# Kernel optimization log

Hardware: AMD Instinct MI355X
Metric: run time of the kernel (lower is better)

## Reference

```python
import jax, jax.numpy as jnp
import numpy as np

B, DIM, H, W = 2, 256, 32, 32
HALF, DI, DS, DTR = DIM // 2, 256, 16, 8
DEPTH, K1 = 2, 4


def _ln(x, w, b, eps=1e-5):
    m = jnp.mean(x, -1, keepdims=True)
    v = jnp.var(x, -1, keepdims=True)
    return (x - m) * jax.lax.rsqrt(v + eps) * w + b


def _selective_scan(dA, dBu, C):
    # dA, dBu: (N, L, D, S); C: (N, L, S) -> y: (N, L, D)
    def step(h, ab):
        a, b = ab
        h = a * h + b
        return h, h
    h0 = jnp.zeros((dA.shape[0],) + dA.shape[2:], dA.dtype)
    _, hs = jax.lax.scan(step, h0, (jnp.moveaxis(dA, 1, 0), jnp.moveaxis(dBu, 1, 0)))
    return jnp.einsum('lnds,nls->nld', hs, C)


def _mamba_block(xs, ln_w, ln_b, in_w, cw, cb, xw, dtw, dtb, Alog, Dp, ow):
    # xs: (B, L, HALF); canonical Mamba-1 block, pre-LN residual
    Lq = xs.shape[1]
    h = _ln(xs, ln_w, ln_b)
    u, z = jnp.split(h @ in_w, 2, axis=-1)  # (B,L,DI) each
    up = jnp.pad(u, ((0, 0), (K1 - 1, 0), (0, 0)))  # causal depthwise conv1d
    u = sum(up[:, k:k + Lq, :] * cw[:, k] for k in range(K1)) + cb
    u = jax.nn.silu(u)
    dbc = u @ xw
    dtr, Bm, Cm = jnp.split(dbc, [DTR, DTR + DS], axis=-1)
    dt = jax.nn.softplus(dtr @ dtw + dtb)  # (B,L,DI)
    A = -jnp.exp(Alog)  # (DI,DS)
    dA = jnp.exp(dt[..., None] * A)
    dBu = (dt * u)[..., None] * Bm[:, :, None, :]
    y = _selective_scan(dA, dBu, Cm) + u * Dp
    return xs + (y * jax.nn.silu(z)) @ ow


def _vss_block(x, ln_w, ln_b, in_w, cw, cb, xw, dtw, dtb, Alog, Dp, on_w, on_b, ow):
    # x: (B, HALF, H, W); VMamba SS2D block (4-direction cross-scan), pre-LN residual
    Bq, _, Hq, Wq = x.shape
    Lq = Hq * Wq
    h = _ln(x.transpose(0, 2, 3, 1), ln_w, ln_b)
    u, z = jnp.split(h @ in_w, 2, axis=-1)  # (B,H,W,DI)
    u2 = jax.lax.conv_general_dilated(u.transpose(0, 3, 1, 2), cw[:, None], (1, 1), ((1, 1), (1, 1)),
                                      feature_group_count=DI,
                                      dimension_numbers=('NCHW', 'OIHW', 'NCHW')) + cb[None, :, None, None]
    u2 = jax.nn.silu(u2)  # (B,DI,H,W)
    s0 = u2.reshape(Bq, DI, Lq)
    s1 = u2.transpose(0, 1, 3, 2).reshape(Bq, DI, Lq)
    us = jnp.stack([s0, s1, jnp.flip(s0, -1), jnp.flip(s1, -1)], 1).transpose(0, 1, 3, 2)  # (B,4,L,DI)
    dbc = jnp.einsum('bkld,kdr->bklr', us, xw)
    dtr, Bm, Cm = jnp.split(dbc, [DTR, DTR + DS], axis=-1)
    dt = jax.nn.softplus(jnp.einsum('bklr,krd->bkld', dtr, dtw) + dtb[None, :, None, :])
    A = -jnp.exp(Alog)  # (4,DI,DS)
    dA = jnp.exp(dt[..., None] * A[None, :, None])  # (B,4,L,DI,DS)
    dBu = (dt * us)[..., None] * Bm[:, :, :, None, :]
    y = _selective_scan(dA.reshape(Bq * 4, Lq, DI, DS), dBu.reshape(Bq * 4, Lq, DI, DS), Cm.reshape(Bq * 4, Lq, DS))
    y = y.reshape(Bq, 4, Lq, DI) + us * Dp[None, :, None, :]
    yt = y.transpose(0, 1, 3, 2)  # (B,4,DI,L)
    y0 = yt[:, 0]
    y1 = yt[:, 1].reshape(Bq, DI, Wq, Hq).transpose(0, 1, 3, 2).reshape(Bq, DI, Lq)
    y2 = jnp.flip(yt[:, 2], -1)
    y3 = jnp.flip(yt[:, 3], -1).reshape(Bq, DI, Wq, Hq).transpose(0, 1, 3, 2).reshape(Bq, DI, Lq)
    ym = _ln((y0 + y1 + y2 + y3).transpose(0, 2, 1), on_w, on_b)  # (B,L,DI)
    out = (ym * jax.nn.silu(z.reshape(Bq, Lq, DI))) @ ow  # (B,L,HALF)
    return x + out.reshape(Bq, Hq, Wq, HALF).transpose(0, 3, 1, 2)


def _fwd(x, proj1_w, proj1_b, proj2_w, proj2_b,
         m_ln_w, m_ln_b, m_in_w, m_conv_w, m_conv_b, m_xproj_w, m_dt_w, m_dt_b, m_Alog, m_D, m_out_w,
         v_ln_w, v_ln_b, v_in_w, v_conv_w, v_conv_b, v_xproj_w, v_dt_w, v_dt_b, v_Alog, v_D,
         v_onorm_w, v_onorm_b, v_out_w, fuse_w, fuse_b, bn_g, bn_b, bn_m, bn_v):
    Bq, _, Hq, Wq = x.shape
    Lq = Hq * Wq
    p1 = jnp.einsum('oc,bchw->bohw', proj1_w, x) + proj1_b[None, :, None, None]
    s = p1.reshape(Bq, HALF, Lq).transpose(0, 2, 1)
    for i in range(DEPTH):
        s = _mamba_block(s, m_ln_w[i], m_ln_b[i], m_in_w[i], m_conv_w[i], m_conv_b[i], m_xproj_w[i],
                         m_dt_w[i], m_dt_b[i], m_Alog[i], m_D[i], m_out_w[i])
    p1 = s.transpose(0, 2, 1).reshape(Bq, HALF, Hq, Wq)
    p2 = jnp.einsum('oc,bchw->bohw', proj2_w, x) + proj2_b[None, :, None, None]
    for i in range(DEPTH):
        p2 = _vss_block(p2, v_ln_w[i], v_ln_b[i], v_in_w[i], v_conv_w[i], v_conv_b[i], v_xproj_w[i],
                        v_dt_w[i], v_dt_b[i], v_Alog[i], v_D[i], v_onorm_w[i], v_onorm_b[i], v_out_w[i])
    xc = jnp.concatenate([p1, p2], 1)
    y = jax.lax.conv_general_dilated(xc, fuse_w, (1, 1), ((1, 1), (1, 1)),
                                     dimension_numbers=('NCHW', 'OIHW', 'NCHW')) + fuse_b[None, :, None, None]
    y = (y - bn_m[None, :, None, None]) * jax.lax.rsqrt(bn_v + 1e-5)[None, :, None, None] * bn_g[None, :, None, None] + bn_b[None, :, None, None]
    return jax.nn.relu(y)


def setup_inputs() -> dict:
    key = jax.random.key(0)
    ks = iter(jax.random.split(key, 64))
    n = lambda shape, s=0.02: jax.random.normal(next(ks), shape, jnp.float32) * s
    A_row = jnp.log(jnp.arange(1, DS + 1, dtype=jnp.float32))  # standard S4D-real init
    return {
        'x': jax.random.normal(next(ks), (B, DIM, H, W), jnp.float32),
        'proj1_w': n((HALF, DIM), 0.05), 'proj1_b': n((HALF,)),
        'proj2_w': n((HALF, DIM), 0.05), 'proj2_b': n((HALF,)),
        'm_ln_w': jnp.ones((DEPTH, HALF)), 'm_ln_b': jnp.zeros((DEPTH, HALF)),
        'm_in_w': n((DEPTH, HALF, 2 * DI)),
        'm_conv_w': n((DEPTH, DI, K1), 0.1), 'm_conv_b': n((DEPTH, DI)),
        'm_xproj_w': n((DEPTH, DI, DTR + 2 * DS)),
        'm_dt_w': n((DEPTH, DTR, DI), 0.1), 'm_dt_b': n((DEPTH, DI)),
        'm_Alog': jnp.array(jnp.broadcast_to(A_row, (DEPTH, DI, DS))),
        'm_D': jnp.ones((DEPTH, DI)),
        'm_out_w': n((DEPTH, DI, HALF)),
        'v_ln_w': jnp.ones((DEPTH, HALF)), 'v_ln_b': jnp.zeros((DEPTH, HALF)),
        'v_in_w': n((DEPTH, HALF, 2 * DI)),
        'v_conv_w': n((DEPTH, DI, 3, 3), 0.1), 'v_conv_b': n((DEPTH, DI)),
        'v_xproj_w': n((DEPTH, 4, DI, DTR + 2 * DS)),
        'v_dt_w': n((DEPTH, 4, DTR, DI), 0.1), 'v_dt_b': n((DEPTH, 4, DI)),
        'v_Alog': jnp.array(jnp.broadcast_to(A_row, (DEPTH, 4, DI, DS))),
        'v_D': jnp.ones((DEPTH, 4, DI)),
        'v_onorm_w': jnp.ones((DEPTH, DI)), 'v_onorm_b': jnp.zeros((DEPTH, DI)),
        'v_out_w': n((DEPTH, DI, HALF)),
        'fuse_w': n((DIM, DIM, 3, 3), 0.02), 'fuse_b': n((DIM,)),
        'bn_g': jnp.ones((DIM,)), 'bn_b': jnp.zeros((DIM,)),
        'bn_m': n((DIM,)), 'bn_v': jax.random.uniform(next(ks), (DIM,), jnp.float32, 0.5, 1.5),
    }


def reference(x, proj1_w, proj1_b, proj2_w, proj2_b,
              m_ln_w, m_ln_b, m_in_w, m_conv_w, m_conv_b, m_xproj_w, m_dt_w, m_dt_b, m_Alog, m_D, m_out_w,
              v_ln_w, v_ln_b, v_in_w, v_conv_w, v_conv_b, v_xproj_w, v_dt_w, v_dt_b, v_Alog, v_D,
              v_onorm_w, v_onorm_b, v_out_w, fuse_w, fuse_b, bn_g, bn_b, bn_m, bn_v):
    return _fwd(x, proj1_w, proj1_b, proj2_w, proj2_b,
                m_ln_w, m_ln_b, m_in_w, m_conv_w, m_conv_b, m_xproj_w, m_dt_w, m_dt_b, m_Alog, m_D, m_out_w,
                v_ln_w, v_ln_b, v_in_w, v_conv_w, v_conv_b, v_xproj_w, v_dt_w, v_dt_b, v_Alog, v_D,
                v_onorm_w, v_onorm_b, v_out_w, fuse_w, fuse_b, bn_g, bn_b, bn_m, bn_v)
```

## Files before the change

### kernel.cpp

```cpp
#include <hip/hip_runtime.h>
#include <math.h>

#define CH  16
#define NCH 64

typedef __attribute__((ext_vector_type(8))) short bf16x8;
typedef __attribute__((ext_vector_type(4))) float f32x4;
typedef __attribute__((ext_vector_type(4))) unsigned int u32x4;

__device__ __forceinline__ float dev_silu(float x){ return x * (1.0f/(1.0f + __expf(-x))); }
__device__ __forceinline__ float dev_softplus(float x){ return fmaxf(x,0.0f) + log1pf(__expf(-fabsf(x))); }
__device__ __forceinline__ unsigned short dev_bf16(float f){
    unsigned int u = __float_as_uint(f);
    return (unsigned short)((u + 0x7fffu + ((u >> 16) & 1u)) >> 16);
}

__global__ void __launch_bounds__(256)
k_prep(const float* __restrict__ w1, const float* __restrict__ w2, float* __restrict__ wtc,
       const float* __restrict__ fw, unsigned short* __restrict__ Wb)
{
    if (blockIdx.x < 64){
        int bc = blockIdx.x;
        int ot = bc & 7, ct = bc >> 3;
        __shared__ float t[32][33];
        int col = threadIdx.x & 31, r8 = threadIdx.x >> 5;
        #pragma unroll
        for (int i = 0; i < 4; ++i){
            int r = i*8 + r8;
            int o = ot*32 + r;
            const float* src = (o < 128) ? (w1 + (size_t)o*256) : (w2 + (size_t)(o-128)*256);
            t[r][col] = src[ct*32 + col];
        }
        __syncthreads();
        #pragma unroll
        for (int i = 0; i < 4; ++i){
            int r = i*8 + r8;
            int c = ct*32 + r, o = ot*32 + col;
            wtc[(size_t)c*256 + o] = t[col][r];
        }
    } else {
        int idx = ((blockIdx.x - 64)*256 + threadIdx.x)*4;
        float4 v = *(const float4*)(fw + idx);
        unsigned int r0 = dev_bf16(v.x), r1 = dev_bf16(v.y), r2 = dev_bf16(v.z), r3 = dev_bf16(v.w);
        uint2 pk; pk.x = r0 | (r1 << 16); pk.y = r2 | (r3 << 16);
        *(uint2*)(Wb + idx) = pk;
    }
}

__global__ void __launch_bounds__(256)
k_proj(const float* __restrict__ x, const float* __restrict__ wtc,
       const float* __restrict__ b1, const float* __restrict__ b2,
       float* __restrict__ sm, float* __restrict__ sv)
{
    int blk = blockIdx.x;
    int b = blk >> 8, l0 = (blk & 255) * 4;
    int tid = threadIdx.x;
    __shared__ float4 xs[256];
    xs[tid] = *(const float4*)(x + ((size_t)(b*256 + tid))*1024 + l0);
    __syncthreads();
    int o = tid & 127;
    float bias = (tid < 128) ? b1[o] : b2[o];
    float a0 = bias, a1 = bias, a2 = bias, a3 = bias;
    #pragma unroll 4
    for (int c = 0; c < 256; ++c){
        float wv = wtc[(size_t)c*256 + tid];
        float4 xv = xs[c];
        a0 = fmaf(wv, xv.x, a0);
        a1 = fmaf(wv, xv.y, a1);
        a2 = fmaf(wv, xv.z, a2);
        a3 = fmaf(wv, xv.w, a3);
    }
    float* dst = (tid < 128) ? sm : sv;
    size_t base = ((size_t)b*1024 + l0)*128 + o;
    dst[base      ] = a0;
    dst[base + 128] = a1;
    dst[base + 256] = a2;
    dst[base + 384] = a3;
}

__device__ __forceinline__ void lnmm_body(int bl0, const float* __restrict__ s,
    const float* __restrict__ lnw, const float* __restrict__ lnb,
    const float* __restrict__ inw, float* __restrict__ u, float* __restrict__ z)
{
    int tid = threadIdx.x;
    int row = tid >> 5, lane = tid & 31;
    __shared__ float hn[8][132];
    float4 v = *(const float4*)(s + (size_t)(bl0 + row)*128 + lane*4);
    float a = v.x + v.y + v.z + v.w;
    float q = v.x*v.x + v.y*v.y + v.z*v.z + v.w*v.w;
    #pragma unroll
    for (int o = 16; o; o >>= 1){ a += __shfl_xor(a, o); q += __shfl_xor(q, o); }
    float mean = a * (1.0f/128.0f);
    float rs = rsqrtf(q * (1.0f/128.0f) - mean*mean + 1e-5f);
    float4 w4 = *(const float4*)(lnw + lane*4);
    float4 b4 = *(const float4*)(lnb + lane*4);
    float4 hv;
    hv.x = (v.x-mean)*rs*w4.x + b4.x;
    hv.y = (v.y-mean)*rs*w4.y + b4.y;
    hv.z = (v.z-mean)*rs*w4.z + b4.z;
    hv.w = (v.w-mean)*rs*w4.w + b4.w;
    *(float4*)&hn[row][lane*4] = hv;
    __syncthreads();
    float acc0[8] = {0,0,0,0,0,0,0,0};
    float acc1[8] = {0,0,0,0,0,0,0,0};
    for (int c = 0; c < 128; c += 4){
        float w0[4], w1[4];
        #pragma unroll
        for (int i = 0; i < 4; ++i){
            w0[i] = inw[(size_t)(c+i)*512 + tid];
            w1[i] = inw[(size_t)(c+i)*512 + tid + 256];
        }
        #pragma unroll
        for (int r = 0; r < 8; ++r){
            float4 h4 = *(const float4*)&hn[r][c];
            acc0[r] = fmaf(h4.x, w0[0], acc0[r]);
            acc0[r] = fmaf(h4.y, w0[1], acc0[r]);
            acc0[r] = fmaf(h4.z, w0[2], acc0[r]);
            acc0[r] = fmaf(h4.w, w0[3], acc0[r]);
            acc1[r] = fmaf(h4.x, w1[0], acc1[r]);
            acc1[r] = fmaf(h4.y, w1[1], acc1[r]);
            acc1[r] = fmaf(h4.z, w1[2], acc1[r]);
            acc1[r] = fmaf(h4.w, w1[3], acc1[r]);
        }
    }
    #pragma unroll
    for (int r = 0; r < 8; ++r){
        u[(size_t)(bl0 + r)*256 + tid] = acc0[r];
        z[(size_t)(bl0 + r)*256 + tid] = acc1[r];
    }
}

__global__ void __launch_bounds__(256)
k_lnmm2(const float* __restrict__ sm_, const float* __restrict__ mlnw, const float* __restrict__ mlnb,
        const float* __restrict__ minw, float* __restrict__ um, float* __restrict__ zm,
        const float* __restrict__ sv_, const float* __restrict__ vlnw, const float* __restrict__ vlnb,
        const float* __restrict__ vinw, float* __restrict__ uv, float* __restrict__ zv)
{
    if (blockIdx.x < 256) lnmm_body(blockIdx.x*8, sm_, mlnw, mlnb, minw, um, zm);
    else                  lnmm_body((blockIdx.x-256)*8, sv_, vlnw, vlnb, vinw, uv, zv);
}

__global__ void __launch_bounds__(256)
k_conv2(const float* __restrict__ urm, const float* __restrict__ cwm, const float* __restrict__ cbm,
        float* __restrict__ uc,
        const float* __restrict__ urv, const float* __restrict__ cwv, const float* __restrict__ cbv,
        float* __restrict__ us)
{
    int d = threadIdx.x;
    if (blockIdx.x < 2048){
        int bl = blockIdx.x; int b = bl >> 10, l = bl & 1023;
        float acc = cbm[d];
        #pragma unroll
        for (int k = 0; k < 4; ++k){
            int lp = l - 3 + k;
            if (lp >= 0) acc = fmaf(urm[((size_t)(b<<10) + lp)*256 + d], cwm[d*4 + k], acc);
        }
        uc[(size_t)bl*256 + d] = dev_silu(acc);
    } else {
        int bl = blockIdx.x - 2048; int b = bl >> 10, l = bl & 1023;
        int h = l >> 5, w = l & 31;
        float acc = cbv[d];
        #pragma unroll
        for (int kh = 0; kh < 3; ++kh){
            int hh = h + kh - 1; if (hh < 0 || hh > 31) continue;
            #pragma unroll
            for (int kw = 0; kw < 3; ++kw){
                int ww = w + kw - 1; if (ww < 0 || ww > 31) continue;
                acc = fmaf(urv[((size_t)(b<<10) + (hh<<5) + ww)*256 + d], cwv[d*9 + kh*3 + kw], acc);
            }
        }
        float v = dev_silu(acc);
        int l1 = (w<<5) + h;
        size_t base = (size_t)b*4*1024*256;
        us[base + ((size_t)0*1024 + l        )*256 + d] = v;
        us[base + ((size_t)1*1024 + l1       )*256 + d] = v;
        us[base + ((size_t)2*1024 + (1023-l ))*256 + d] = v;
        us[base + ((size_t)3*1024 + (1023-l1))*256 + d] = v;
    }
}

__device__ __forceinline__ void xproj_body(size_t idx0, int k, const float* __restrict__ u,
    const float* __restrict__ xw, const float* __restrict__ dtw, const float* __restrict__ dtb,
    float* __restrict__ dt, float* __restrict__ Bm, float* __restrict__ Cm)
{
    int tid = threadIdx.x;
    __shared__ float ursh[4][256];
    __shared__ float dbc[4][44];
    #pragma unroll
    for (int p = 0; p < 4; ++p)
        ursh[p][tid] = u[(idx0 + p)*256 + tid];
    __syncthreads();
    if (tid < 160){
        int r = tid % 40, p = tid / 40;
        const float* xwc = xw + (size_t)k*256*40 + r;
        float a0 = 0.f, a1 = 0.f;
        for (int c = 0; c < 128; ++c){
            a0 = fmaf(ursh[p][c],       xwc[(size_t)c*40],       a0);
            a1 = fmaf(ursh[p][c + 128], xwc[(size_t)(c+128)*40], a1);
        }
        dbc[p][r] = a0 + a1;
    }
    __syncthreads();
    const float* dtwk = dtw + (size_t)k*8*256;
    float bias = dtb[k*256 + tid];
    float wv[8];
    #pragma unroll
    for (int r = 0; r < 8; ++r) wv[r] = dtwk[r*256 + tid];
    #pragma unroll
    for (int p = 0; p < 4; ++p){
        float a = bias;
        #pragma unroll
        for (int r = 0; r < 8; ++r) a = fmaf(dbc[p][r], wv[r], a);
        dt[(idx0 + p)*256 + tid] = dev_softplus(a);
    }
    if (tid < 128){
        int p = tid >> 5, j = tid & 31;
        if (j < 16) Bm[(idx0 + p)*16 + j]        = dbc[p][8 + j];
        else        Cm[(idx0 + p)*16 + (j - 16)] = dbc[p][8 + j];
    }
}

__global__ void __launch_bounds__(256)
k_xproj2(const float* __restrict__ um, const float* __restrict__ mxw, const float* __restrict__ mdtw,
         const float* __restrict__ mdtb, float* __restrict__ dtm, float* __restrict__ Bmm,
         float* __restrict__ Cmm,
         const float* __restrict__ uv, const float* __restrict__ vxw, const float* __restrict__ vdtw,
         const float* __restrict__ vdtb, float* __restrict__ dtv, float* __restrict__ Bmv,
         float* __restrict__ Cmv)
{
    if (blockIdx.x < 512){
        int bk = blockIdx.x >> 8;
        size_t idx0 = (size_t)bk*1024 + (blockIdx.x & 255)*4;
        xproj_body(idx0, 0, um, mxw, mdtw, mdtb, dtm, Bmm, Cmm);
    } else {
        int blk = blockIdx.x - 512;
        int bk = blk >> 8;
        size_t idx0 = (size_t)bk*1024 + (blk & 255)*4;
        xproj_body(idx0, bk & 3, uv, vxw, vdtw, vdtb, dtv, Bmv, Cmv);
    }
}

__device__ __forceinline__ void scanA_body(int bk, int c, int k, const float* __restrict__ dt,
    const float* __restrict__ u, const float* __restrict__ Bm, const float* __restrict__ Alog,
    float* __restrict__ Pb, float* __restrict__ Qb)
{
    int d = threadIdx.x;
    __shared__ float Bsh[CH][16];
    {
        int j = threadIdx.x >> 4, s = threadIdx.x & 15;
        Bsh[j][s] = Bm[((size_t)bk*1024 + c*CH + j)*16 + s];
    }
    float dtv[CH], duv[CH];
    size_t base = ((size_t)bk*1024 + c*CH)*256 + d;
    #pragma unroll
    for (int j = 0; j < CH; ++j){
        float a = dt[base + (size_t)j*256];
        float b = u [base + (size_t)j*256];
        dtv[j] = a; duv[j] = a*b;
    }
    float A[16];
    const float4* Ap = (const float4*)(Alog + ((size_t)k*256 + d)*16);
    #pragma unroll
    for (int q = 0; q < 4; ++q){
        float4 v = Ap[q];
        A[q*4+0] = -__expf(v.x); A[q*4+1] = -__expf(v.y);
        A[q*4+2] = -__expf(v.z); A[q*4+3] = -__expf(v.w);
    }
    __syncthreads();
    float Q[16];
    #pragma unroll
    for (int s = 0; s < 16; ++s) Q[s] = 0.f;
    float S = 0.f;
    #pragma unroll
    for (int j = 0; j < CH; ++j){
        S += dtv[j];
        #pragma unroll
        for (int s = 0; s < 16; ++s){
            float av = __expf(dtv[j]*A[s]);
            Q[s] = fmaf(av, Q[s], duv[j]*Bsh[j][s]);
        }
    }
    size_t oidx = ((size_t)(bk*NCH + c)*256 + d)*16;
    float4* Pp = (float4*)(Pb + oidx);
    float4* Qp = (float4*)(Qb + oidx);
    #pragma unroll
    for (int q = 0; q < 4; ++q){
        float4 pv, qv;
        pv.x = __expf(S*A[q*4+0]); pv.y = __expf(S*A[q*4+1]);
        pv.z = __expf(S*A[q*4+2]); pv.w = __expf(S*A[q*4+3]);
        qv.x = Q[q*4+0]; qv.y = Q[q*4+1]; qv.z = Q[q*4+2]; qv.w = Q[q*4+3];
        Pp[q] = pv; Qp[q] = qv;
    }
}

__global__ void __launch_bounds__(256)
k_scanA2(const float* __restrict__ dtm, const float* __restrict__ um, const float* __restrict__ Bmm,
         const float* __restrict__ mAlog, float* __restrict__ Pbm, float* __restrict__ Qbm,
         const float* __restrict__ dtv, const float* __restrict__ uv, const float* __restrict__ Bmv,
         const float* __restrict__ vAlog, float* __restrict__ Pbv, float* __restrict__ Qbv)
{
    if (blockIdx.x < 128){
        int blk = blockIdx.x;
        scanA_body(blk >> 6, blk & (NCH-1), 0, dtm, um, Bmm, mAlog, Pbm, Qbm);
    } else {
        int blk = blockIdx.x - 128;
        int bk = blk >> 6;
        scanA_body(bk, blk & (NCH-1), bk & 3, dtv, uv, Bmv, vAlog, Pbv, Qbv);
    }
}

__device__ __forceinline__ void scanP_body(int bk, int dg, float* __restrict__ Pb,
                                           const float* __restrict__ Qb)
{
    int tid = threadIdx.x;
    size_t idx0 = (size_t)bk*NCH*4096 + dg*256 + tid;
    float Pv[NCH], Qv[NCH];
    #pragma unroll
    for (int c = 0; c < NCH; ++c){
        Pv[c] = Pb[idx0 + (size_t)c*4096];
        Qv[c] = Qb[idx0 + (size_t)c*4096];
    }
    float h = 0.f;
    #pragma unroll
    for (int c = 0; c < NCH; ++c){
        Pb[idx0 + (size_t)c*4096] = h;
        h = fmaf(Pv[c], h, Qv[c]);
    }
}

__global__ void __launch_bounds__(256)
k_scanP2(float* __restrict__ Pbm, const float* __restrict__ Qbm,
         float* __restrict__ Pbv, const float* __restrict__ Qbv)
{
    if (blockIdx.x < 32) scanP_body(blockIdx.x >> 4, blockIdx.x & 15, Pbm, Qbm);
    else { int blk = blockIdx.x - 32; scanP_body(blk >> 4, blk & 15, Pbv, Qbv); }
}

__device__ __forceinline__ void scanB_body(int bk, int c, int k, const float* __restrict__ dt,
    const float* __restrict__ u, const float* __restrict__ Bm, const float* __restrict__ Cm,
    const float* __restrict__ Alog, const float* __restrict__ Hb, float* __restrict__ y)
// ... 34 lines not shown
    #pragma unroll
    for (int j = 0; j < CH; ++j){
        float py = 0.f;
        #pragma unroll
        for (int s = 0; s < 16; ++s){
            float av = __expf(dtv[j]*A[s]);
            h[s] = fmaf(av, h[s], duv[j]*Bsh[j][s]);
            py = fmaf(h[s], Csh[j][s], py);
        }
        yp[(size_t)j*256] = py;
    }
}

__global__ void __launch_bounds__(256)
k_scanB2(const float* __restrict__ dtm, const float* __restrict__ um, const float* __restrict__ Bmm,
         const float* __restrict__ Cmm, const float* __restrict__ mAlog,
         const float* __restrict__ Hbm, float* __restrict__ ym,
         const float* __restrict__ dtv, const float* __restrict__ uv, const float* __restrict__ Bmv,
         const float* __restrict__ Cmv, const float* __restrict__ vAlog,
         const float* __restrict__ Hbv, float* __restrict__ yv)
{
    if (blockIdx.x < 128){
        int blk = blockIdx.x;
        scanB_body(blk >> 6, blk & (NCH-1), 0, dtm, um, Bmm, Cmm, mAlog, Hbm, ym);
    } else {
        int blk = blockIdx.x - 128;
        int bk = blk >> 6;
        scanB_body(bk, blk & (NCH-1), bk & 3, dtv, uv, Bmv, Cmv, vAlog, Hbv, yv);
    }
}

__device__ __forceinline__ void mout_body(int bl0, const float* __restrict__ y,
    const float* __restrict__ uc, const float* __restrict__ z, const float* __restrict__ Dp,
    const float* __restrict__ ow, float* __restrict__ sm)
{
    int tid = threadIdx.x;
    int row = tid >> 5, c0 = (tid & 31) * 8;
    __shared__ float gld[8][264];
    size_t base = (size_t)(bl0 + row)*256 + c0;
    #pragma unroll
    for (int i = 0; i < 8; i += 4){
        float4 yv = *(const float4*)(y + base + i);
        float4 uv = *(const float4*)(uc + base + i);
        float4 zv = *(const float4*)(z + base + i);
        float4 dv = *(const float4*)(Dp + c0 + i);
        gld[row][c0+i+0] = (yv.x + uv.x*dv.x) * dev_silu(zv.x);
        gld[row][c0+i+1] = (yv.y + uv.y*dv.y) * dev_silu(zv.y);
        gld[row][c0+i+2] = (yv.z + uv.z*dv.z) * dev_silu(zv.z);
        gld[row][c0+i+3] = (yv.w + uv.w*dv.w) * dev_silu(zv.w);
    }
    __syncthreads();
    int o = tid & 127, rg = tid >> 7;
    float acc[4] = {0,0,0,0};
    for (int c = 0; c < 256; c += 4){
        float w[4];
        #pragma unroll
        for (int i = 0; i < 4; ++i) w[i] = ow[(size_t)(c+i)*128 + o];
        #pragma unroll
        for (int r = 0; r < 4; ++r){
            float4 h4 = *(const float4*)&gld[rg*4 + r][c];
            acc[r] = fmaf(h4.x, w[0], acc[r]);
            acc[r] = fmaf(h4.y, w[1], acc[r]);
            acc[r] = fmaf(h4.z, w[2], acc[r]);
            acc[r] = fmaf(h4.w, w[3], acc[r]);
        }
    }
    #pragma unroll
    for (int r = 0; r < 4; ++r)
        sm[(size_t)(bl0 + rg*4 + r)*128 + o] += acc[r];
}

__device__ __forceinline__ void vcomb_body(int blk, const float* __restrict__ y,
    const float* __restrict__ us, const float* __restrict__ z, const float* __restrict__ Dp,
    const float* __restrict__ onw, const float* __restrict__ onb, const float* __restrict__ ow,
    float* __restrict__ sv)
{
    int b = blk >> 7;
    int l0 = (blk & 127) * 8;
    int tid = threadIdx.x;
    int row = tid >> 5, c0 = (tid & 31) * 8;
    int l = l0 + row;
    int h = l >> 5, w = l & 31;
    int l1 = (w<<5) + h, l2 = 1023 - l, l3 = 1023 - l1;
    size_t base = (size_t)b*4*1024*256;
    size_t i0 = base + ((size_t)0*1024 + l )*256 + c0;
    size_t i1 = base + ((size_t)1*1024 + l1)*256 + c0;
    size_t i2 = base + ((size_t)2*1024 + l2)*256 + c0;
    size_t i3 = base + ((size_t)3*1024 + l3)*256 + c0;
    float t[8];
    #pragma unroll
    for (int i = 0; i < 8; i += 4){
        float4 yv = *(const float4*)(y + i0 + i);
        float4 uv = *(const float4*)(us + i0 + i);
        float4 dv = *(const float4*)(Dp + 0*256 + c0 + i);
        t[i+0] = yv.x + uv.x*dv.x; t[i+1] = yv.y + uv.y*dv.y;
        t[i+2] = yv.z + uv.z*dv.z; t[i+3] = yv.w + uv.w*dv.w;
    }
    #pragma unroll
    for (int i = 0; i < 8; i += 4){
        float4 yv = *(const float4*)(y + i1 + i);
        float4 uv = *(const float4*)(us + i1 + i);
        float4 dv = *(const float4*)(Dp + 1*256 + c0 + i);
        t[i+0] += yv.x + uv.x*dv.x; t[i+1] += yv.y + uv.y*dv.y;
        t[i+2] += yv.z + uv.z*dv.z; t[i+3] += yv.w + uv.w*dv.w;
    }
    #pragma unroll
    for (int i = 0; i < 8; i += 4){
        float4 yv = *(const float4*)(y + i2 + i);
// ... 16 lines not shown
    #pragma unroll
    for (int o = 16; o; o >>= 1){ a += __shfl_xor(a, o); q += __shfl_xor(q, o); }
    float mean = a * (1.0f/256.0f);
    float rs = rsqrtf(q * (1.0f/256.0f) - mean*mean + 1e-5f);
    __shared__ float gld[8][264];
    size_t zbase = (size_t)(b*1024 + l)*256 + c0;
    #pragma unroll
    for (int i = 0; i < 8; i += 4){
        float4 wv = *(const float4*)(onw + c0 + i);
        float4 bv = *(const float4*)(onb + c0 + i);
        float4 zv = *(const float4*)(z + zbase + i);
        gld[row][c0+i+0] = ((t[i+0]-mean)*rs*wv.x + bv.x) * dev_silu(zv.x);
        gld[row][c0+i+1] = ((t[i+1]-mean)*rs*wv.y + bv.y) * dev_silu(zv.y);
        gld[row][c0+i+2] = ((t[i+2]-mean)*rs*wv.z + bv.z) * dev_silu(zv.z);
        gld[row][c0+i+3] = ((t[i+3]-mean)*rs*wv.w + bv.w) * dev_silu(zv.w);
    }
    __syncthreads();
    int o = tid & 127, rg = tid >> 7;
    float acc[4] = {0,0,0,0};
    for (int c = 0; c < 256; c += 4){
        float wv[4];
        #pragma unroll
        for (int i = 0; i < 4; ++i) wv[i] = ow[(size_t)(c+i)*128 + o];
        #pragma unroll
        for (int r = 0; r < 4; ++r){
            float4 h4 = *(const float4*)&gld[rg*4 + r][c];
            acc[r] = fmaf(h4.x, wv[0], acc[r]);
            acc[r] = fmaf(h4.y, wv[1], acc[r]);
            acc[r] = fmaf(h4.z, wv[2], acc[r]);
            acc[r] = fmaf(h4.w, wv[3], acc[r]);
        }
    }
    #pragma unroll
    for (int r = 0; r < 4; ++r)
        sv[(size_t)(b*1024 + l0 + rg*4 + r)*128 + o] += acc[r];
}

__global__ void __launch_bounds__(256)
k_epi2(const float* __restrict__ ym, const float* __restrict__ uc, const float* __restrict__ zm,
       const float* __restrict__ mD, const float* __restrict__ mow, float* __restrict__ sm,
       const float* __restrict__ yv, const float* __restrict__ us, const float* __restrict__ zv,
       const float* __restrict__ vD, const float* __restrict__ onw, const float* __restrict__ onb,
       const float* __restrict__ vow, float* __restrict__ sv)
{
    if (blockIdx.x < 256) mout_body(blockIdx.x*8, ym, uc, zm, mD, mow, sm);
    else                  vcomb_body(blockIdx.x-256, yv, us, zv, vD, onw, onb, vow, sv);
}

__global__ void __launch_bounds__(256)
k_im2col(const float* __restrict__ sm, const float* __restrict__ sv,
         unsigned short* __restrict__ Bt)
{
    int n = blockIdx.x; int b = n >> 10, p = n & 1023;
    int h = p >> 5, w = p & 31;
    int tid = threadIdx.x;
    #pragma unroll
    for (int it = 0; it < 9; ++it){
        int k = it*256 + tid;
        int c = k / 9, r = k - c*9;
        int kh = r / 3, kw = r - kh*3;
        int hh = h + kh - 1, ww = w + kw - 1;
        float v = 0.f;
        if (hh >= 0 && hh < 32 && ww >= 0 && ww < 32){
            int l = (hh << 5) + ww;
            v = (c < 128) ? sm[((size_t)b*1024 + l)*128 + c]
                          : sv[((size_t)b*1024 + l)*128 + (c - 128)];
        }
        Bt[(size_t)n*2304 + k] = dev_bf16(v);
    }
}

__global__ void __launch_bounds__(256)
k_fgemm(const unsigned short* __restrict__ Wb, const unsigned short* __restrict__ Bt,
        const float* __restrict__ fb, const float* __restrict__ bg, const float* __restrict__ bb,
        const float* __restrict__ bm, const float* __restrict__ bv, float* __restrict__ out)
{
    int o0 = (blockIdx.x & 3) * 64;
    int n0 = (blockIdx.x >> 2) * 64;
    int tid = threadIdx.x, lane = tid & 63, wid = tid >> 6;
    int wm = (wid >> 1) * 32, wn = (wid & 1) * 32;
    __shared__ unsigned short sA[64*40];
    __shared__ unsigned short sB[64*40];
    f32x4 acc[2][2] = {};
    int srow = tid >> 2, scol = (tid & 3) * 8;
    const u32x4* gA = (const u32x4*)(Wb + (size_t)(o0 + srow)*2304 + scol);
    const u32x4* gB = (const u32x4*)(Bt + (size_t)(n0 + srow)*2304 + scol);
    u32x4* wA = (u32x4*)(sA + srow*40 + scol);
    u32x4* wB = (u32x4*)(sB + srow*40 + scol);
    int fr = lane & 15, fk = (lane >> 4) * 8;
    const unsigned short* rA0 = sA + (wm + fr)*40 + fk;
    const unsigned short* rA1 = sA + (wm + 16 + fr)*40 + fk;
    const unsigned short* rB0 = sB + (wn + fr)*40 + fk;
    const unsigned short* rB1 = sB + (wn + 16 + fr)*40 + fk;
    for (int kt = 0; kt < 72; ++kt){
        u32x4 va = gA[kt*4];
        u32x4 vb = gB[kt*4];
        __syncthreads();
        *wA = va; *wB = vb;
        __syncthreads();
        bf16x8 a0 = *(const bf16x8*)rA0;
        bf16x8 a1 = *(const bf16x8*)rA1;
        bf16x8 b0 = *(const bf16x8*)rB0;
        bf16x8 b1 = *(const bf16x8*)rB1;
        acc[0][0] = __builtin_amdgcn_mfma_f32_16x16x32_bf16(a0, b0, acc[0][0], 0, 0, 0);
        acc[0][1] = __builtin_amdgcn_mfma_f32_16x16x32_bf16(a0, b1, acc[0][1], 0, 0, 0);
        acc[1][0] = __builtin_amdgcn_mfma_f32_16x16x32_bf16(a1, b0, acc[1][0], 0, 0, 0);
        acc[1][1] = __builtin_amdgcn_mfma_f32_16x16x32_bf16(a1, b1, acc[1][1], 0, 0, 0);
    }
    #pragma unroll
    for (int i = 0; i < 2; ++i){
        int ob = o0 + wm + i*16 + (lane >> 4) * 4;
        #pragma unroll
        for (int j = 0; j < 2; ++j){
            int n = n0 + wn + j*16 + (lane & 15);
            int b = n >> 10, p = n & 1023;
            #pragma unroll
            for (int q = 0; q < 4; ++q){
                int o = ob + q;
                float v = acc[i][j][q] + fb[o];
                v = (v - bm[o]) * rsqrtf(bv[o] + 1e-5f) * bg[o] + bb[o];
                out[((size_t)(b*256 + o))*1024 + p] = fmaxf(v, 0.f);
            }
        }
    }
}

extern "C" void kernel_launch(void* const* d_in, const int* in_sizes, int n_in,
                              void* d_out, int out_size, void* d_ws, size_t ws_size,
                              hipStream_t stream)
{
    const float* x         = (const float*)d_in[0];
    const float* proj1_w   = (const float*)d_in[1];
    const float* proj1_b   = (const float*)d_in[2];
    const float* proj2_w   = (const float*)d_in[3];
    const float* proj2_b   = (const float*)d_in[4];
    const float* m_ln_w    = (const float*)d_in[5];
    const float* m_ln_b    = (const float*)d_in[6];
    const float* m_in_w    = (const float*)d_in[7];
    const float* m_conv_w  = (const float*)d_in[8];
    const float* m_conv_b  = (const float*)d_in[9];
    const float* m_xproj_w = (const float*)d_in[10];
    const float* m_dt_w    = (const float*)d_in[11];
    const float* m_dt_b    = (const float*)d_in[12];
    const float* m_Alog    = (const float*)d_in[13];
    const float* m_D       = (const float*)d_in[14];
    const float* m_out_w   = (const float*)d_in[15];
    const float* v_ln_w    = (const float*)d_in[16];
    const float* v_ln_b    = (const float*)d_in[17];
    const float* v_in_w    = (const float*)d_in[18];
    const float* v_conv_w  = (const float*)d_in[19];
    const float* v_conv_b  = (const float*)d_in[20];
    const float* v_xproj_w = (const float*)d_in[21];
    const float* v_dt_w    = (const float*)d_in[22];
    const float* v_dt_b    = (const float*)d_in[23];
// ... 2 lines not shown
    const float* v_onorm_w = (const float*)d_in[26];
    const float* v_onorm_b = (const float*)d_in[27];
    const float* v_out_w   = (const float*)d_in[28];
    const float* fuse_w    = (const float*)d_in[29];
    const float* fuse_b    = (const float*)d_in[30];
    const float* bn_g      = (const float*)d_in[31];
    const float* bn_b      = (const float*)d_in[32];
    const float* bn_m      = (const float*)d_in[33];
    const float* bn_v      = (const float*)d_in[34];
    float* out = (float*)d_out;

    float* ws = (float*)d_ws;
    float* sm     = ws;  ws += 2*1024*128;
    float* sv     = ws;  ws += 2*1024*128;
    float* uraw_m = ws;  ws += 2*1024*256;
    float* zb_m   = ws;  ws += 2*1024*256;
    float* uc     = ws;  ws += 2*1024*256;
    float* uraw_v = ws;  ws += 2*1024*256;
    float* zb_v   = ws;  ws += 2*1024*256;
    float* usb    = ws;  ws += 2*4*1024*256;
    float* dt_m   = ws;  ws += 2*1024*256;
    float* yb_m   = ws;  ws += 2*1024*256;
    float* Pb_m   = ws;  ws += 2*NCH*256*16;
    float* Qb_m   = ws;  ws += 2*NCH*256*16;
    float* Bm_m   = ws;  ws += 2*1024*16;
    float* Cm_m   = ws;  ws += 2*1024*16;
    float* dt_v   = ws;  ws += 2*4*1024*256;
    float* yb_v   = ws;  ws += 2*4*1024*256;
    float* Pb_v   = ws;  ws += 2*4*NCH*256*16;
    float* Qb_v   = ws;  ws += 2*4*NCH*256*16;
    float* Bm_v   = ws;  ws += 2*4*1024*16;
    float* Cm_v   = ws;  ws += 2*4*1024*16;
    float* wtc    = ws;  ws += 256*256;
    unsigned short* Wbf = (unsigned short*)ws;  ws += 576*1024/2;
    unsigned short* Bmat = (unsigned short*)dt_v;

    k_prep<<<640,   256, 0, stream>>>(proj1_w, proj2_w, wtc, fuse_w, Wbf);
    k_proj<<<2*256, 256, 0, stream>>>(x, wtc, proj1_b, proj2_b, sm, sv);

    for (int i = 0; i < 2; ++i){
        k_lnmm2 <<<512,  256, 0, stream>>>(sm, m_ln_w + i*128, m_ln_b + i*128,
                                           m_in_w + (size_t)i*65536, uraw_m, zb_m,
                                           sv, v_ln_w + i*128, v_ln_b + i*128,
                                           v_in_w + (size_t)i*65536, uraw_v, zb_v);
        k_conv2 <<<4096, 256, 0, stream>>>(uraw_m, m_conv_w + (size_t)i*1024, m_conv_b + i*256, uc,
                                           uraw_v, v_conv_w + (size_t)i*2304, v_conv_b + i*256, usb);
        k_xproj2<<<2560, 256, 0, stream>>>(uc,  m_xproj_w + (size_t)i*10240,
                                           m_dt_w + (size_t)i*2048, m_dt_b + i*256,
                                           dt_m, Bm_m, Cm_m,
                                           usb, v_xproj_w + (size_t)i*40960,
                                           v_dt_w + (size_t)i*8192, v_dt_b + (size_t)i*1024,
                                           dt_v, Bm_v, Cm_v);
        k_scanA2<<<640,  256, 0, stream>>>(dt_m, uc,  Bm_m, m_Alog + (size_t)i*4096,  Pb_m, Qb_m,
                                           dt_v, usb, Bm_v, v_Alog + (size_t)i*16384, Pb_v, Qb_v);
        k_scanP2<<<160,  256, 0, stream>>>(Pb_m, Qb_m, Pb_v, Qb_v);
        k_scanB2<<<640,  256, 0, stream>>>(dt_m, uc,  Bm_m, Cm_m, m_Alog + (size_t)i*4096,
                                           Pb_m, yb_m,
                                           dt_v, usb, Bm_v, Cm_v, v_Alog + (size_t)i*16384,
                                           Pb_v, yb_v);
        k_epi2  <<<512,  256, 0, stream>>>(yb_m, uc, zb_m, m_D + i*256,
                                           m_out_w + (size_t)i*32768, sm,
                                           yb_v, usb, zb_v, v_D + (size_t)i*1024,
                                           v_onorm_w + i*256, v_onorm_b + i*256,
                                           v_out_w + (size_t)i*32768, sv);
    }

    k_im2col<<<2*1024, 256, 0, stream>>>(sm, sv, Bmat);
    k_fgemm <<<4*32,   256, 0, stream>>>(Wbf, Bmat, fuse_b, bn_g, bn_b, bn_m, bn_v, out);
}
```

Baseline: 297.1 us.

## Fuse x-proj into scan pass A, epilogue into next LN+in-proj, im2col into GEMM

```diff
diff --git a/kernel.cpp b/kernel.cpp
--- a/kernel.cpp
+++ b/kernel.cpp
@@ -17,7 +17,7 @@
 
 __global__ void __launch_bounds__(256)
 k_prep(const float* __restrict__ w1, const float* __restrict__ w2, float* __restrict__ wtc,
-       const float* __restrict__ fw, unsigned short* __restrict__ Wb)
+       const float* __restrict__ fw, unsigned short* __restrict__ Wr)
 {
     if (blockIdx.x < 64){
         int bc = blockIdx.x;
@@ -39,11 +39,17 @@
             wtc[(size_t)c*256 + o] = t[col][r];
         }
     } else {
-        int idx = ((blockIdx.x - 64)*256 + threadIdx.x)*4;
-        float4 v = *(const float4*)(fw + idx);
-        unsigned int r0 = dev_bf16(v.x), r1 = dev_bf16(v.y), r2 = dev_bf16(v.z), r3 = dev_bf16(v.w);
-        uint2 pk; pk.x = r0 | (r1 << 16); pk.y = r2 | (r3 << 16);
-        *(uint2*)(Wb + idx) = pk;
+        int t0 = ((blockIdx.x - 64)*256 + threadIdx.x)*4;
+        unsigned int r[4];
+        #pragma unroll
+        for (int j = 0; j < 4; ++j){
+            int i = t0 + j;
+            int o = i / 2304, kk = i - o*2304;
+            int kp = kk >> 8, cc = kk & 255;
+            r[j] = dev_bf16(fw[(size_t)o*2304 + cc*9 + kp]);
+        }
+        uint2 pk; pk.x = r[0] | (r[1] << 16); pk.y = r[2] | (r[3] << 16);
+        *(uint2*)(Wr + t0) = pk;
     }
 }
 
@@ -78,14 +84,13 @@
     dst[base + 384] = a3;
 }
 
-__device__ __forceinline__ void lnmm_body(int bl0, const float* __restrict__ s,
+__device__ __forceinline__ void lnmm_core(int bl0, float4 v,
     const float* __restrict__ lnw, const float* __restrict__ lnb,
-    const float* __restrict__ inw, float* __restrict__ u, float* __restrict__ z)
+    const float* __restrict__ inw, float* __restrict__ u, float* __restrict__ z,
+    float (*hn)[132])
 {
     int tid = threadIdx.x;
     int row = tid >> 5, lane = tid & 31;
-    __shared__ float hn[8][132];
-    float4 v = *(const float4*)(s + (size_t)(bl0 + row)*128 + lane*4);
     float a = v.x + v.y + v.z + v.w;
     float q = v.x*v.x + v.y*v.y + v.z*v.z + v.w*v.w;
     #pragma unroll
@@ -136,8 +141,18 @@
         const float* __restrict__ sv_, const float* __restrict__ vlnw, const float* __restrict__ vlnb,
         const float* __restrict__ vinw, float* __restrict__ uv, float* __restrict__ zv)
 {
-    if (blockIdx.x < 256) lnmm_body(blockIdx.x*8, sm_, mlnw, mlnb, minw, um, zm);
-    else                  lnmm_body((blockIdx.x-256)*8, sv_, vlnw, vlnb, vinw, uv, zv);
+    __shared__ float hn[8][132];
+    int tid = threadIdx.x;
+    int row = tid >> 5, lane = tid & 31;
+    if (blockIdx.x < 256){
+        int bl0 = blockIdx.x*8;
+        float4 v = *(const float4*)(sm_ + (size_t)(bl0 + row)*128 + lane*4);
+        lnmm_core(bl0, v, mlnw, mlnb, minw, um, zm, hn);
+    } else {
+        int bl0 = (blockIdx.x-256)*8;
+        float4 v = *(const float4*)(sv_ + (size_t)(bl0 + row)*128 + lane*4);
+        lnmm_core(bl0, v, vlnw, vlnb, vinw, uv, zv, hn);
+    }
 }
 
 __global__ void __launch_bounds__(256)
@@ -179,26 +194,52 @@
     }
 }
 
-__device__ __forceinline__ void xproj_body(size_t idx0, int k, const float* __restrict__ u,
-    const float* __restrict__ xw, const float* __restrict__ dtw, const float* __restrict__ dtb,
-    float* __restrict__ dt, float* __restrict__ Bm, float* __restrict__ Cm)
+__device__ __forceinline__ void xsa_body(int bk, int ch, int k,
+    const float* __restrict__ u, const float* __restrict__ xw,
+    const float* __restrict__ dtw, const float* __restrict__ dtb,
+    const float* __restrict__ Alog,
+    float* __restrict__ dt, float* __restrict__ Bm, float* __restrict__ Cm,
+    float* __restrict__ Pb, float* __restrict__ Qb)
 {
     int tid = threadIdx.x;
-    __shared__ float ursh[4][256];
-    __shared__ float dbc[4][44];
-    #pragma unroll
-    for (int p = 0; p < 4; ++p)
+    __shared__ float ursh[16][256];
+    __shared__ float xwsh[64][40];
+    __shared__ float dbc[16][44];
+    size_t idx0 = (size_t)bk*1024 + ch*CH;
+    #pragma unroll
+    for (int p = 0; p < 16; ++p)
         ursh[p][tid] = u[(idx0 + p)*256 + tid];
+    const float* xwk = xw + (size_t)k*256*40;
+    int pp[3], rr[3];
+    #pragma unroll
+    for (int rnd = 0; rnd < 3; ++rnd){
+        int t = rnd*256 + tid;
+        pp[rnd] = t/40; rr[rnd] = t - pp[rnd]*40;
+    }
+    float accd[3] = {0.f, 0.f, 0.f};
+    for (int ct = 0; ct < 4; ++ct){
+        __syncthreads();
+        for (int i = tid; i < 64*40; i += 256)
+            xwsh[i/40][i%40] = xwk[(size_t)(ct*64 + i/40)*40 + (i%40)];
+        __syncthreads();
+        #pragma unroll
+        for (int rnd = 0; rnd < 3; ++rnd){
+            int t = rnd*256 + tid;
+            if (t < 640){
+                int p = pp[rnd], r = rr[rnd];
+                float a = accd[rnd];
+                #pragma unroll 8
+                for (int cc = 0; cc < 64; ++cc)
+                    a = fmaf(ursh[p][ct*64 + cc], xwsh[cc][r], a);
+                accd[rnd] = a;
+            }
+        }
+    }
     __syncthreads();
-    if (tid < 160){
-        int r = tid % 40, p = tid / 40;
-        const float* xwc = xw + (size_t)k*256*40 + r;
-        float a0 = 0.f, a1 = 0.f;
-        for (int c = 0; c < 128; ++c){
-            a0 = fmaf(ursh[p][c],       xwc[(size_t)c*40],       a0);
-            a1 = fmaf(ursh[p][c + 128], xwc[(size_t)(c+128)*40], a1);
-        }
-        dbc[p][r] = a0 + a1;
+    #pragma unroll
+    for (int rnd = 0; rnd < 3; ++rnd){
+        int t = rnd*256 + tid;
+        if (t < 640) dbc[pp[rnd]][rr[rnd]] = accd[rnd];
     }
     __syncthreads();
     const float* dtwk = dtw + (size_t)k*8*256;
@@ -206,81 +247,44 @@
     float wv[8];
     #pragma unroll
     for (int r = 0; r < 8; ++r) wv[r] = dtwk[r*256 + tid];
-    #pragma unroll
-    for (int p = 0; p < 4; ++p){
+    float dtv[16], duv[16];
+    #pragma unroll
+    for (int p = 0; p < 16; ++p){
         float a = bias;
         #pragma unroll
         for (int r = 0; r < 8; ++r) a = fmaf(dbc[p][r], wv[r], a);
-        dt[(idx0 + p)*256 + tid] = dev_softplus(a);
-    }
-    if (tid < 128){
-        int p = tid >> 5, j = tid & 31;
-        if (j < 16) Bm[(idx0 + p)*16 + j]        = dbc[p][8 + j];
-        else        Cm[(idx0 + p)*16 + (j - 16)] = dbc[p][8 + j];
-    }
-}
-
-__global__ void __launch_bounds__(256)
-k_xproj2(const float* __restrict__ um, const float* __restrict__ mxw, const float* __restrict__ mdtw,
-         const float* __restrict__ mdtb, float* __restrict__ dtm, float* __restrict__ Bmm,
-         float* __restrict__ Cmm,
-         const float* __restrict__ uv, const float* __restrict__ vxw, const float* __restrict__ vdtw,
-         const float* __restrict__ vdtb, float* __restrict__ dtv, float* __restrict__ Bmv,
-         float* __restrict__ Cmv)
-{
-    if (blockIdx.x < 512){
-        int bk = blockIdx.x >> 8;
-        size_t idx0 = (size_t)bk*1024 + (blockIdx.x & 255)*4;
-        xproj_body(idx0, 0, um, mxw, mdtw, mdtb, dtm, Bmm, Cmm);
-    } else {
-        int blk = blockIdx.x - 512;
-        int bk = blk >> 8;
-        size_t idx0 = (size_t)bk*1024 + (blk & 255)*4;
-        xproj_body(idx0, bk & 3, uv, vxw, vdtw, vdtb, dtv, Bmv, Cmv);
-    }
-}
-
-__device__ __forceinline__ void scanA_body(int bk, int c, int k, const float* __restrict__ dt,
-    const float* __restrict__ u, const float* __restrict__ Bm, const float* __restrict__ Alog,
-    float* __restrict__ Pb, float* __restrict__ Qb)
-{
-    int d = threadIdx.x;
-    __shared__ float Bsh[CH][16];
+        a = dev_softplus(a);
+        dtv[p] = a;
+        dt[(idx0 + p)*256 + tid] = a;
+        duv[p] = a * ursh[p][tid];
+    }
     {
-        int j = threadIdx.x >> 4, s = threadIdx.x & 15;
-        Bsh[j][s] = Bm[((size_t)bk*1024 + c*CH + j)*16 + s];
-    }
-    float dtv[CH], duv[CH];
-    size_t base = ((size_t)bk*1024 + c*CH)*256 + d;
-    #pragma unroll
-    for (int j = 0; j < CH; ++j){
-        float a = dt[base + (size_t)j*256];
-        float b = u [base + (size_t)j*256];
-        dtv[j] = a; duv[j] = a*b;
+        int p = tid >> 4, s = tid & 15;
+        Bm[(idx0 + p)*16 + s] = dbc[p][8 + s];
+        Cm[(idx0 + p)*16 + s] = dbc[p][24 + s];
     }
     float A[16];
-    const float4* Ap = (const float4*)(Alog + ((size_t)k*256 + d)*16);
+    const float4* Ap = (const float4*)(Alog + ((size_t)k*256 + tid)*16);
     #pragma unroll
     for (int q = 0; q < 4; ++q){
         float4 v = Ap[q];
         A[q*4+0] = -__expf(v.x); A[q*4+1] = -__expf(v.y);
         A[q*4+2] = -__expf(v.z); A[q*4+3] = -__expf(v.w);
     }
-    __syncthreads();
     float Q[16];
     #pragma unroll
     for (int s = 0; s < 16; ++s) Q[s] = 0.f;
     float S = 0.f;
     #pragma unroll
-    for (int j = 0; j < CH; ++j){
+    for (int j = 0; j < 16; ++j){
         S += dtv[j];
         #pragma unroll
         for (int s = 0; s < 16; ++s){
             float av = __expf(dtv[j]*A[s]);
-            Q[s] = fmaf(av, Q[s], duv[j]*Bsh[j][s]);
-        }
-    }
-    size_t oidx = ((size_t)(bk*NCH + c)*256 + d)*16;
+            Q[s] = fmaf(av, Q[s], duv[j]*dbc[j][8 + s]);
+        }
+    }
+    size_t oidx = ((size_t)(bk*NCH + ch)*256 + tid)*16;
     float4* Pp = (float4*)(Pb + oidx);
     float4* Qp = (float4*)(Qb + oidx);
     #pragma unroll
@@ -294,18 +298,22 @@
 }
 
 __global__ void __launch_bounds__(256)
-k_scanA2(const float* __restrict__ dtm, const float* __restrict__ um, const float* __restrict__ Bmm,
-         const float* __restrict__ mAlog, float* __restrict__ Pbm, float* __restrict__ Qbm,
-         const float* __restrict__ dtv, const float* __restrict__ uv, const float* __restrict__ Bmv,
-         const float* __restrict__ vAlog, float* __restrict__ Pbv, float* __restrict__ Qbv)
+k_xsa2(const float* __restrict__ um, const float* __restrict__ mxw, const float* __restrict__ mdtw,
+       const float* __restrict__ mdtb, const float* __restrict__ mAlog,
+       float* __restrict__ dtm, float* __restrict__ Bmm, float* __restrict__ Cmm,
+       float* __restrict__ Pbm, float* __restrict__ Qbm,
+       const float* __restrict__ uv, const float* __restrict__ vxw, const float* __restrict__ vdtw,
+       const float* __restrict__ vdtb, const float* __restrict__ vAlog,
+       float* __restrict__ dtv_, float* __restrict__ Bmv, float* __restrict__ Cmv,
+       float* __restrict__ Pbv, float* __restrict__ Qbv)
 {
     if (blockIdx.x < 128){
         int blk = blockIdx.x;
-        scanA_body(blk >> 6, blk & (NCH-1), 0, dtm, um, Bmm, mAlog, Pbm, Qbm);
+        xsa_body(blk >> 6, blk & 63, 0, um, mxw, mdtw, mdtb, mAlog, dtm, Bmm, Cmm, Pbm, Qbm);
     } else {
         int blk = blockIdx.x - 128;
         int bk = blk >> 6;
-        scanA_body(bk, blk & (NCH-1), bk & 3, dtv, uv, Bmv, vAlog, Pbv, Qbv);
+        xsa_body(bk, blk & 63, bk & 3, uv, vxw, vdtw, vdtb, vAlog, dtv_, Bmv, Cmv, Pbv, Qbv);
     }
 }
 
@@ -406,7 +414,7 @@
 
 __device__ __forceinline__ void mout_body(int bl0, const float* __restrict__ y,
     const float* __restrict__ uc, const float* __restrict__ z, const float* __restrict__ Dp,
-    const float* __restrict__ ow, float* __restrict__ sm)
+    const float* __restrict__ ow, float* __restrict__ sm, float* __restrict__ srowp)
 {
     int tid = threadIdx.x;
     int row = tid >> 5, c0 = (tid & 31) * 8;
@@ -440,14 +448,18 @@
         }
     }
     #pragma unroll
-    for (int r = 0; r < 4; ++r)
-        sm[(size_t)(bl0 + rg*4 + r)*128 + o] += acc[r];
+    for (int r = 0; r < 4; ++r){
+        size_t gi = (size_t)(bl0 + rg*4 + r)*128 + o;
+        float nv = sm[gi] + acc[r];
+        sm[gi] = nv;
+        srowp[(rg*4 + r)*128 + o] = nv;
+    }
 }
 
 __device__ __forceinline__ void vcomb_body(int blk, const float* __restrict__ y,
     const float* __restrict__ us, const float* __restrict__ z, const float* __restrict__ Dp,
     const float* __restrict__ onw, const float* __restrict__ onb, const float* __restrict__ ow,
-    float* __restrict__ sv)
+    float* __restrict__ sv, float* __restrict__ srowp)
 {
     int b = blk >> 7;
     int l0 = (blk & 127) * 8;
@@ -530,8 +542,12 @@
         }
     }
     #pragma unroll
-    for (int r = 0; r < 4; ++r)
-        sv[(size_t)(b*1024 + l0 + rg*4 + r)*128 + o] += acc[r];
+    for (int r = 0; r < 4; ++r){
+        size_t gi = (size_t)(b*1024 + l0 + rg*4 + r)*128 + o;
+        float nv = sv[gi] + acc[r];
+        sv[gi] = nv;
+        srowp[(rg*4 + r)*128 + o] = nv;
+    }
 }
 
 __global__ void __launch_bounds__(256)
@@ -541,36 +557,46 @@
        const float* __restrict__ vD, const float* __restrict__ onw, const float* __restrict__ onb,
        const float* __restrict__ vow, float* __restrict__ sv)
 {
-    if (blockIdx.x < 256) mout_body(blockIdx.x*8, ym, uc, zm, mD, mow, sm);
-    else                  vcomb_body(blockIdx.x-256, yv, us, zv, vD, onw, onb, vow, sv);
-}
-
-__global__ void __launch_bounds__(256)
-k_im2col(const float* __restrict__ sm, const float* __restrict__ sv,
-         unsigned short* __restrict__ Bt)
-{
-    int n = blockIdx.x; int b = n >> 10, p = n & 1023;
-    int h = p >> 5, w = p & 31;
+    __shared__ float srow[8][128];
+    if (blockIdx.x < 256) mout_body(blockIdx.x*8, ym, uc, zm, mD, mow, sm, &srow[0][0]);
+    else                  vcomb_body(blockIdx.x-256, yv, us, zv, vD, onw, onb, vow, sv, &srow[0][0]);
+}
+
+__global__ void __launch_bounds__(256)
+k_epln2(const float* __restrict__ ym, const float* __restrict__ uc, const float* __restrict__ zm,
+        const float* __restrict__ mD, const float* __restrict__ mow, float* __restrict__ sm,
+        const float* __restrict__ yv, const float* __restrict__ us, const float* __restrict__ zv,
+        const float* __restrict__ vD, const float* __restrict__ onw, const float* __restrict__ onb,
+        const float* __restrict__ vow, float* __restrict__ sv,
+        const float* __restrict__ mlnw, const float* __restrict__ mlnb, const float* __restrict__ minw,
+        float* __restrict__ um_o, float* __restrict__ zm_o,
+        const float* __restrict__ vlnw, const float* __restrict__ vlnb, const float* __restrict__ vinw,
+        float* __restrict__ uv_o, float* __restrict__ zv_o)
+{
+    __shared__ float srow[8][128];
+    __shared__ float hn[8][132];
     int tid = threadIdx.x;
-    #pragma unroll
-    for (int it = 0; it < 9; ++it){
-        int k = it*256 + tid;
-        int c = k / 9, r = k - c*9;
-        int kh = r / 3, kw = r - kh*3;
-        int hh = h + kh - 1, ww = w + kw - 1;
-        float v = 0.f;
-        if (hh >= 0 && hh < 32 && ww >= 0 && ww < 32){
-            int l = (hh << 5) + ww;
-            v = (c < 128) ? sm[((size_t)b*1024 + l)*128 + c]
-                          : sv[((size_t)b*1024 + l)*128 + (c - 128)];
-        }
-        Bt[(size_t)n*2304 + k] = dev_bf16(v);
-    }
-}
-
-__global__ void __launch_bounds__(256)
-k_fgemm(const unsigned short* __restrict__ Wb, const unsigned short* __restrict__ Bt,
-        const float* __restrict__ fb, const float* __restrict__ bg, const float* __restrict__ bb,
+    int row = tid >> 5, lane = tid & 31;
+    if (blockIdx.x < 256){
+        int bl0 = blockIdx.x*8;
+        mout_body(bl0, ym, uc, zm, mD, mow, sm, &srow[0][0]);
+        __syncthreads();
+        float4 v = *(const float4*)&srow[row][lane*4];
+        lnmm_core(bl0, v, mlnw, mlnb, minw, um_o, zm_o, hn);
+    } else {
+        int blk = blockIdx.x - 256;
+        int bl0 = (blk >> 7)*1024 + (blk & 127)*8;
+        vcomb_body(blk, yv, us, zv, vD, onw, onb, vow, sv, &srow[0][0]);
+        __syncthreads();
+        float4 v = *(const float4*)&srow[row][lane*4];
+        lnmm_core(bl0, v, vlnw, vlnb, vinw, uv_o, zv_o, hn);
+    }
+}
+
+__global__ void __launch_bounds__(256)
+k_fgemm(const unsigned short* __restrict__ Wr, const float* __restrict__ sm,
+        const float* __restrict__ sv, const float* __restrict__ fb,
+        const float* __restrict__ bg, const float* __restrict__ bb,
         const float* __restrict__ bm, const float* __restrict__ bv, float* __restrict__ out)
 {
     int o0 = (blockIdx.x & 3) * 64;
@@ -581,10 +607,10 @@
     __shared__ unsigned short sB[64*40];
     f32x4 acc[2][2] = {};
     int srow = tid >> 2, scol = (tid & 3) * 8;
-    const u32x4* gA = (const u32x4*)(Wb + (size_t)(o0 + srow)*2304 + scol);
-    const u32x4* gB = (const u32x4*)(Bt + (size_t)(n0 + srow)*2304 + scol);
+    const u32x4* gA = (const u32x4*)(Wr + (size_t)(o0 + srow)*2304 + scol);
     u32x4* wA = (u32x4*)(sA + srow*40 + scol);
     u32x4* wB = (u32x4*)(sB + srow*40 + scol);
+    int n = n0 + srow; int b = n >> 10, p = n & 1023, h = p >> 5, w = p & 31;
     int fr = lane & 15, fk = (lane >> 4) * 8;
     const unsigned short* rA0 = sA + (wm + fr)*40 + fk;
     const unsigned short* rA1 = sA + (wm + 16 + fr)*40 + fk;
@@ -592,7 +618,22 @@
     const unsigned short* rB1 = sB + (wn + 16 + fr)*40 + fk;
     for (int kt = 0; kt < 72; ++kt){
         u32x4 va = gA[kt*4];
-        u32x4 vb = gB[kt*4];
+        int kp = kt >> 3, c0 = (kt & 7) * 32;
+        int kh = kp / 3, kw = kp - kh*3;
+        int hh = h + kh - 1, ww = w + kw - 1;
+        int cg = c0 + scol;
+        float4 v0 = make_float4(0.f,0.f,0.f,0.f), v1 = v0;
+        if ((unsigned)hh < 32u && (unsigned)ww < 32u){
+            const float* sp = ((cg < 128) ? sm : sv)
+                            + ((size_t)(b*1024 + (hh<<5) + ww))*128 + (cg & 127);
+            v0 = *(const float4*)sp;
+            v1 = *(const float4*)(sp + 4);
+        }
+        u32x4 vb;
+        vb.x = dev_bf16(v0.x) | ((unsigned)dev_bf16(v0.y) << 16);
+        vb.y = dev_bf16(v0.z) | ((unsigned)dev_bf16(v0.w) << 16);
+        vb.z = dev_bf16(v1.x) | ((unsigned)dev_bf16(v1.y) << 16);
+        vb.w = dev_bf16(v1.z) | ((unsigned)dev_bf16(v1.w) << 16);
         __syncthreads();
         *wA = va; *wB = vb;
         __syncthreads();
@@ -610,14 +651,14 @@
         int ob = o0 + wm + i*16 + (lane >> 4) * 4;
         #pragma unroll
         for (int j = 0; j < 2; ++j){
-            int n = n0 + wn + j*16 + (lane & 15);
-            int b = n >> 10, p = n & 1023;
+            int nn = n0 + wn + j*16 + (lane & 15);
+            int bb_ = nn >> 10, pp = nn & 1023;
             #pragma unroll
             for (int q = 0; q < 4; ++q){
                 int o = ob + q;
                 float v = acc[i][j][q] + fb[o];
                 v = (v - bm[o]) * rsqrtf(bv[o] + 1e-5f) * bg[o] + bb[o];
-                out[((size_t)(b*256 + o))*1024 + p] = fmaxf(v, 0.f);
+                out[((size_t)(bb_*256 + o))*1024 + pp] = fmaxf(v, 0.f);
             }
         }
     }
@@ -686,39 +727,45 @@
     float* Bm_v   = ws;  ws += 2*4*1024*16;
     float* Cm_v   = ws;  ws += 2*4*1024*16;
     float* wtc    = ws;  ws += 256*256;
-    unsigned short* Wbf = (unsigned short*)ws;  ws += 576*1024/2;
-    unsigned short* Bmat = (unsigned short*)dt_v;
-
-    k_prep<<<640,   256, 0, stream>>>(proj1_w, proj2_w, wtc, fuse_w, Wbf);
+    unsigned short* Wr = (unsigned short*)ws;  ws += 576*1024/2;
+
+    k_prep<<<640,   256, 0, stream>>>(proj1_w, proj2_w, wtc, fuse_w, Wr);
     k_proj<<<2*256, 256, 0, stream>>>(x, wtc, proj1_b, proj2_b, sm, sv);
 
+    k_lnmm2<<<512, 256, 0, stream>>>(sm, m_ln_w, m_ln_b, m_in_w, uraw_m, zb_m,
+                                     sv, v_ln_w, v_ln_b, v_in_w, uraw_v, zb_v);
+
     for (int i = 0; i < 2; ++i){
-        k_lnmm2 <<<512,  256, 0, stream>>>(sm, m_ln_w + i*128, m_ln_b + i*128,
-                                           m_in_w + (size_t)i*65536, uraw_m, zb_m,
-                                           sv, v_ln_w + i*128, v_ln_b + i*128,
-                                           v_in_w + (size_t)i*65536, uraw_v, zb_v);
         k_conv2 <<<4096, 256, 0, stream>>>(uraw_m, m_conv_w + (size_t)i*1024, m_conv_b + i*256, uc,
                                            uraw_v, v_conv_w + (size_t)i*2304, v_conv_b + i*256, usb);
-        k_xproj2<<<2560, 256, 0, stream>>>(uc,  m_xproj_w + (size_t)i*10240,
+        k_xsa2  <<<640,  256, 0, stream>>>(uc,  m_xproj_w + (size_t)i*10240,
                                            m_dt_w + (size_t)i*2048, m_dt_b + i*256,
-                                           dt_m, Bm_m, Cm_m,
+                                           m_Alog + (size_t)i*4096,
+                                           dt_m, Bm_m, Cm_m, Pb_m, Qb_m,
                                            usb, v_xproj_w + (size_t)i*40960,
                                            v_dt_w + (size_t)i*8192, v_dt_b + (size_t)i*1024,
-                                           dt_v, Bm_v, Cm_v);
-        k_scanA2<<<640,  256, 0, stream>>>(dt_m, uc,  Bm_m, m_Alog + (size_t)i*4096,  Pb_m, Qb_m,
-                                           dt_v, usb, Bm_v, v_Alog + (size_t)i*16384, Pb_v, Qb_v);
+                                           v_Alog + (size_t)i*16384,
+                                           dt_v, Bm_v, Cm_v, Pb_v, Qb_v);
         k_scanP2<<<160,  256, 0, stream>>>(Pb_m, Qb_m, Pb_v, Qb_v);
         k_scanB2<<<640,  256, 0, stream>>>(dt_m, uc,  Bm_m, Cm_m, m_Alog + (size_t)i*4096,
                                            Pb_m, yb_m,
                                            dt_v, usb, Bm_v, Cm_v, v_Alog + (size_t)i*16384,
                                            Pb_v, yb_v);
-        k_epi2  <<<512,  256, 0, stream>>>(yb_m, uc, zb_m, m_D + i*256,
-                                           m_out_w + (size_t)i*32768, sm,
-                                           yb_v, usb, zb_v, v_D + (size_t)i*1024,
-                                           v_onorm_w + i*256, v_onorm_b + i*256,
-                                           v_out_w + (size_t)i*32768, sv);
-    }
-
-    k_im2col<<<2*1024, 256, 0, stream>>>(sm, sv, Bmat);
-    k_fgemm <<<4*32,   256, 0, stream>>>(Wbf, Bmat, fuse_b, bn_g, bn_b, bn_m, bn_v, out);
-}
+        if (i == 0){
+            k_epln2<<<512, 256, 0, stream>>>(yb_m, uc, zb_m, m_D, m_out_w, sm,
+                                             yb_v, usb, zb_v, v_D,
+                                             v_onorm_w, v_onorm_b, v_out_w, sv,
+                                             m_ln_w + 128, m_ln_b + 128, m_in_w + 65536,
+                                             uraw_m, zb_m,
+                                             v_ln_w + 128, v_ln_b + 128, v_in_w + 65536,
+                                             uraw_v, zb_v);
+        } else {
+            k_epi2 <<<512, 256, 0, stream>>>(yb_m, uc, zb_m, m_D + 256, m_out_w + 32768, sm,
+                                             yb_v, usb, zb_v, v_D + 1024,
+                                             v_onorm_w + 256, v_onorm_b + 256,
+                                             v_out_w + 32768, sv);
+        }
+    }
+
+    k_fgemm<<<4*32, 256, 0, stream>>>(Wr, sm, sv, fuse_b, bn_g, bn_b, bn_m, bn_v, out);
+}
```

After: 351.2 us. +18.2%, slower.
